# Optimization experiments

Measured on AMD Instinct MI355X. Metric: run time of the kernel, lower is better.

## Reference

```python
import jax, jax.numpy as jnp
from jax import lax
import numpy as np

B, H, W_, C, F = 4, 32, 32, 16, 16
KH, KW = 3, 3
L = 1.0


def setup_inputs() -> dict:
    key = jax.random.key(0)
    k1, k2, k3, k4 = jax.random.split(key, 4)
    inputs = jax.random.normal(k1, (B, H, W_, C), dtype=jnp.float32)
    # lecun_normal-style scales (stddev = 1/sqrt(fan_in))
    m_scale = 1.0 / np.sqrt(H * W_ * 1)
    g_scale = 1.0 / np.sqrt(KH * KW * C)
    M = jax.random.normal(k2, (H, W_, 1, H, W_, 1), dtype=jnp.float32) * m_scale
    Wp = jax.random.normal(k3, (H, W_, 1, H, W_, 1), dtype=jnp.float32) * m_scale
    G = jax.random.normal(k4, (H, W_, KH, KW, C, F), dtype=jnp.float32) * g_scale
    return {"inputs": inputs, "M": M, "Wp": Wp, "G": G}


def reference(inputs, M, Wp, G):
    b, h, w, c = inputs.shape
    kh, kw, f = G.shape[2], G.shape[3], G.shape[5]
    M2 = M[:, :, 0, :, :, 0]   # (i,j,p,q)
    W2 = Wp[:, :, 0, :, :, 0]  # (i,j,p,q)
    # first_term[b,i,j,c] = sum_pq M[i,j,p,q] * inputs[b,p,q,c]
    first = jnp.einsum('ijpq,bpqc->bijc', M2, inputs)
    # One big conv: kernel (kh,kw,c, h*w*f) gives shifted for every output pixel (i,j)
    K = jnp.transpose(G, (2, 3, 4, 0, 1, 5)).reshape(kh, kw, c, h * w * f)
    shifted = lax.conv_general_dilated(
        inputs, K, window_strides=(1, 1), padding='SAME',
        dimension_numbers=('NHWC', 'HWIO', 'NHWC'))
    shifted = shifted.reshape(b, h, w, h, w, f)  # (b,p,q,i,j,f)
    diff = jax.nn.relu(inputs[:, :, :, None, None, :] - shifted)  # (b,p,q,i,j,c)
    # second_term[b,i,j,c] = sum_pq W[i,j,p,q] * relu(inputs - shifted)[b,p,q,i,j,c]
    second = jnp.einsum('ijpq,bpqijc->bijc', W2, diff)
    return first - L * second
```

## Files before the change

### kernel.cpp

```cpp
#include <hip/hip_runtime.h>


typedef __attribute__((ext_vector_type(8))) short bf16x8;
typedef __attribute__((ext_vector_type(4))) float f32x4;

__device__ inline unsigned short f2bf(float x) {
    unsigned u = __float_as_uint(x);
    u += 0x7FFFu + ((u >> 16) & 1u);
    return (unsigned short)(u >> 16);
}
__device__ inline unsigned pack2(float a, float b) {
    return (unsigned)f2bf(a) | ((unsigned)f2bf(b) << 16);
}

template<bool XF>
__global__ __launch_bounds__(256) void build_A(const float* __restrict__ inp,
                                               uint4* __restrict__ A,
                                               float4* __restrict__ Xf) {
    const int tid = blockIdx.x * 256 + threadIdx.x;
    const int u = tid >> 12;
    if (XF && u >= 20) {
        const int idx = tid - 81920;
        const int tile = idx >> 6;
        const int ll = idx & 63;
        const int rowb = tile * 16 + (ll >> 4) * 4;
        const int col = ll & 15;
        float4 v;
        v.x = inp[(rowb + 0) * 16 + col];
        v.y = inp[(rowb + 1) * 16 + col];
        v.z = inp[(rowb + 2) * 16 + col];
        v.w = inp[(rowb + 3) * 16 + col];
        Xf[idx] = v;
        return;
    }
    const int row = tid & 4095;
    const int tile = row >> 4, m = row & 15;
    if (u >= 18) {
        const uint4 z = {0, 0, 0, 0};
        A[(tile * 5 + 4) * 64 + (u - 16) * 16 + m] = z;
        return;
    }
    const int tap = u >> 1, h = u & 1;
    const int dh = tap / 3, dw = tap - dh * 3;
    const int b = row >> 10, pq = row & 1023;
    const int p = pq >> 5, q = pq & 31;
    const int pp = p + dh - 1, qq = q + dw - 1;
    const int kk = tap >> 1, quad = (tap & 1) * 2 + h;
    uint4 o = {0, 0, 0, 0};
    if (((unsigned)pp < 32u) && ((unsigned)qq < 32u)) {
        const float4* s = (const float4*)(inp + b * 16384 + (pp * 32 + qq) * 16 + 8 * h);
        const float4 f0 = s[0], f1 = s[1];
        o.x = pack2(f0.x, f0.y); o.y = pack2(f0.z, f0.w);
        o.z = pack2(f1.x, f1.y); o.w = pack2(f1.z, f1.w);
    }
    A[(tile * 5 + kk) * 64 + quad * 16 + m] = o;
}

template<bool XF>
__global__ __launch_bounds__(512, 2) void inrf_main(
    const float* __restrict__ inp,
    const float* __restrict__ M,
    const float* __restrict__ Wp,
    const float* __restrict__ G,
    const uint4* __restrict__ Aw,
    const float4* __restrict__ Xf,
    float* __restrict__ out)
{
    const int bid = blockIdx.x;
    const int t = threadIdx.x;

    __shared__ __align__(16) float W2l[4096];
    __shared__ __align__(16) float M2l[4096];
    __shared__ float red[8][64];

    {
        const float* Wg = Wp + bid * 4096;
        const float* Mg = M  + bid * 4096;
#pragma unroll
        for (int i = 0; i < 8; ++i) {
            W2l[t + i * 512] = Wg[t + i * 512];
            M2l[t + i * 512] = Mg[t + i * 512];
        }
    }

    const int l = t & 63, w = t >> 6;
    const int quad = l >> 4, col = l & 15;
    const int b = w >> 1;

    const float* Gg = G + bid * 9216;
    bf16x8 Bf[4][5];
#pragma unroll
    for (int ij = 0; ij < 4; ++ij) {
#pragma unroll
        for (int kk = 0; kk < 5; ++kk) {
            bf16x8 f;
#pragma unroll
            for (int j = 0; j < 8; ++j) {
                const int k = kk * 32 + quad * 8 + j;
                const float v = (k < 144) ? Gg[ij * 2304 + k * 16 + col] : 0.f;
                f[j] = (short)f2bf(v);
            }
            Bf[ij][kk] = f;
        }
    }

    __syncthreads();

    const int tile0 = b * 64 + (w & 1) * 32;
    const float* inb = inp + b * 16384;
    (void)inb;

    float accv[4] = {0.f, 0.f, 0.f, 0.f};

    uint4 A0[5], A1[5];
    float4 v0, v1;

    auto prefetch = [&](uint4 (&Ar)[5], float4& vr, int tn) {
#pragma unroll
        for (int kk = 0; kk < 5; ++kk) Ar[kk] = Aw[(tn * 5 + kk) * 64 + l];
        if (XF) {
            vr = Xf[tn * 64 + l];
        } else {
            const int pqb = (tn & 63) * 16 + quad * 4;
            vr.x = inb[(pqb + 0) * 16 + col];
            vr.y = inb[(pqb + 1) * 16 + col];
            vr.z = inb[(pqb + 2) * 16 + col];
            vr.w = inb[(pqb + 3) * 16 + col];
        }
    };

    auto compute = [&](const uint4 (&Ar)[5], const float4& vr, int tg) {
        f32x4 C[4];
#pragma unroll
        for (int ij = 0; ij < 4; ++ij) C[ij] = (f32x4){0.f, 0.f, 0.f, 0.f};
#pragma unroll
        for (int kk = 0; kk < 5; ++kk) {
            const bf16x8 a = __builtin_bit_cast(bf16x8, Ar[kk]);
#pragma unroll
            for (int ij = 0; ij < 4; ++ij)
                C[ij] = __builtin_amdgcn_mfma_f32_16x16x32_bf16(a, Bf[ij][kk], C[ij], 0, 0, 0);
        }
        const int pqb = (tg & 63) * 16 + quad * 4;
#pragma unroll
        for (int ij = 0; ij < 4; ++ij) {
            const float4 w2 = *(const float4*)&W2l[ij * 1024 + pqb];
            const float4 m2 = *(const float4*)&M2l[ij * 1024 + pqb];
            accv[ij] += m2.x * vr.x - w2.x * fmaxf(vr.x - C[ij][0], 0.f);
            accv[ij] += m2.y * vr.y - w2.y * fmaxf(vr.y - C[ij][1], 0.f);
            accv[ij] += m2.z * vr.z - w2.z * fmaxf(vr.z - C[ij][2], 0.f);
            accv[ij] += m2.w * vr.w - w2.w * fmaxf(vr.w - C[ij][3], 0.f);
        }
    };

    prefetch(A0, v0, tile0);
#pragma unroll 1
    for (int i = 0; i < 32; i += 2) {
        prefetch(A1, v1, tile0 + i + 1);
        compute(A0, v0, tile0 + i);
        if (i + 2 < 32) prefetch(A0, v0, tile0 + i + 2);
        compute(A1, v1, tile0 + i + 1);
    }

#pragma unroll
    for (int ij = 0; ij < 4; ++ij) {
        float v = accv[ij];
        v += __shfl_xor(v, 16);
        v += __shfl_xor(v, 32);
        if (l < 16) red[w][ij * 16 + l] = v;
    }
    __syncthreads();

    if (t < 256) {
        const int ob = t >> 6, oij = (t >> 4) & 3, oc = t & 15;
        const float r0 = red[ob * 2][oij * 16 + oc] + red[ob * 2 + 1][oij * 16 + oc];
        out[ob * 16384 + (bid * 4 + oij) * 16 + oc] = r0;
    }
}

extern "C" void kernel_launch(void* const* d_in, const int* in_sizes, int n_in,
                              void* d_out, int out_size, void* d_ws, size_t ws_size,
                              hipStream_t stream) {
    const float* inp = (const float*)d_in[0];
    const float* M   = (const float*)d_in[1];
    const float* Wp  = (const float*)d_in[2];
    const float* G   = (const float*)d_in[3];
    float* out = (float*)d_out;

    uint4*  A  = (uint4*)d_ws;
    float4* Xf = (float4*)((char*)d_ws + 81920 * sizeof(uint4));
    const size_t need = 81920 * sizeof(uint4) + 16384 * sizeof(float4);

    if (ws_size >= need) {
        build_A<true><<<dim3(384), dim3(256), 0, stream>>>(inp, A, Xf);
        inrf_main<true><<<dim3(256), dim3(512), 0, stream>>>(inp, M, Wp, G, A, Xf, out);
    } else {
        build_A<false><<<dim3(320), dim3(256), 0, stream>>>(inp, A, nullptr);
        inrf_main<false><<<dim3(256), dim3(512), 0, stream>>>(inp, M, Wp, G, A, nullptr, out);
    }
}
```

Baseline: 98.31 us.

## Repartition work: blocks own ij-slices and tile groups, stage A via LDS, atomic reduce

Each block now handles 64 output pixels (8 per wave) across a group of 16 pq-tiles, rather than 4 pixels across all tiles. Shared A tiles and input values are double-buffered in LDS with global_load_lds, so all 8 waves reuse them instead of each loading from global. M and Wp are read straight from global rather than staged in LDS. Partial sums go to out with atomicAdd, so build_A now zeroes the output first. The workspace-size fallback path is dropped. The atomics and the doubled B-fragment register footprint may reduce occupancy or add contention.

```diff
diff --git a/kernel.cpp b/kernel.cpp
--- a/kernel.cpp
+++ b/kernel.cpp
@@ -13,13 +13,22 @@
     return (unsigned)f2bf(a) | ((unsigned)f2bf(b) << 16);
 }
 
-template<bool XF>
+__device__ inline void gld_lds16(const void* g, void* l) {
+    __builtin_amdgcn_global_load_lds((const __attribute__((address_space(1))) void*)g,
+                                     (__attribute__((address_space(3))) void*)l, 16, 0, 0);
+}
+
 __global__ __launch_bounds__(256) void build_A(const float* __restrict__ inp,
                                                uint4* __restrict__ A,
-                                               float4* __restrict__ Xf) {
+                                               float4* __restrict__ Xf,
+                                               float4* __restrict__ outz) {
     const int tid = blockIdx.x * 256 + threadIdx.x;
     const int u = tid >> 12;
-    if (XF && u >= 20) {
+    if (u >= 24) {
+        outz[tid - 98304] = (float4){0.f, 0.f, 0.f, 0.f};
+        return;
+    }
+    if (u >= 20) {
         const int idx = tid - 81920;
         const int tile = idx >> 6;
         const int ll = idx & 63;
@@ -56,9 +65,7 @@
     A[(tile * 5 + kk) * 64 + quad * 16 + m] = o;
 }
 
-template<bool XF>
 __global__ __launch_bounds__(512, 2) void inrf_main(
-    const float* __restrict__ inp,
     const float* __restrict__ M,
     const float* __restrict__ Wp,
     const float* __restrict__ G,
@@ -67,113 +74,106 @@
     float* __restrict__ out)
 {
     const int bid = blockIdx.x;
-    const int t = threadIdx.x;
+    const int ijblk = bid & 15;
+    const int tgrp  = bid >> 4;
+    const int tile0 = tgrp * 16;
+    const int bb    = tile0 >> 6;
 
-    __shared__ __align__(16) float W2l[4096];
-    __shared__ __align__(16) float M2l[4096];
-    __shared__ float red[8][64];
+    const int t = threadIdx.x, l = t & 63, w = t >> 6;
+    const int quad = l >> 4, col = l & 15;
 
-    {
-        const float* Wg = Wp + bid * 4096;
-        const float* Mg = M  + bid * 4096;
+    __shared__ __align__(16) uint4  Ab[2][4][5][64];
+    __shared__ __align__(16) float4 Xb[2][4][64];
+
+    auto stage = [&](int buf, int ct0) {
 #pragma unroll
-        for (int i = 0; i < 8; ++i) {
-            W2l[t + i * 512] = Wg[t + i * 512];
-            M2l[t + i * 512] = Mg[t + i * 512];
+        for (int r = 0; r < 3; ++r) {
+            const int s = w * 3 + r;
+            if (s < 20) {
+                const int ct = s / 5, kk = s - ct * 5;
+                gld_lds16(&Aw[((ct0 + ct) * 5 + kk) * 64 + l], &Ab[buf][ct][kk][0]);
+            } else {
+                const int ct = s - 20;
+                gld_lds16(&Xf[(ct0 + ct) * 64 + l], &Xb[buf][ct][0]);
+            }
         }
-    }
+    };
 
-    const int l = t & 63, w = t >> 6;
-    const int quad = l >> 4, col = l & 15;
-    const int b = w >> 1;
+    stage(0, tile0);
 
-    const float* Gg = G + bid * 9216;
-    bf16x8 Bf[4][5];
+    const int ij0 = ijblk * 64 + w * 8;
+    bf16x8 Bf[8][5];
 #pragma unroll
-    for (int ij = 0; ij < 4; ++ij) {
+    for (int ij = 0; ij < 8; ++ij) {
+        const float* Gg = G + (ij0 + ij) * 2304;
 #pragma unroll
         for (int kk = 0; kk < 5; ++kk) {
             bf16x8 f;
 #pragma unroll
             for (int j = 0; j < 8; ++j) {
                 const int k = kk * 32 + quad * 8 + j;
-                const float v = (k < 144) ? Gg[ij * 2304 + k * 16 + col] : 0.f;
+                const float v = (k < 144) ? Gg[k * 16 + col] : 0.f;
                 f[j] = (short)f2bf(v);
             }
             Bf[ij][kk] = f;
         }
     }
 
+    float accv[8] = {0.f, 0.f, 0.f, 0.f, 0.f, 0.f, 0.f, 0.f};
+
+    asm volatile("s_waitcnt vmcnt(0)" ::: "memory");
     __syncthreads();
 
-    const int tile0 = b * 64 + (w & 1) * 32;
-    const float* inb = inp + b * 16384;
-    (void)inb;
-
-    float accv[4] = {0.f, 0.f, 0.f, 0.f};
-
-    uint4 A0[5], A1[5];
-    float4 v0, v1;
-
-    auto prefetch = [&](uint4 (&Ar)[5], float4& vr, int tn) {
+    int buf = 0;
+#pragma unroll 1
+    for (int ph = 0; ph < 4; ++ph) {
+        if (ph < 3) stage(buf ^ 1, tile0 + (ph + 1) * 4);
 #pragma unroll
-        for (int kk = 0; kk < 5; ++kk) Ar[kk] = Aw[(tn * 5 + kk) * 64 + l];
-        if (XF) {
-            vr = Xf[tn * 64 + l];
-        } else {
-            const int pqb = (tn & 63) * 16 + quad * 4;
-            vr.x = inb[(pqb + 0) * 16 + col];
-            vr.y = inb[(pqb + 1) * 16 + col];
-            vr.z = inb[(pqb + 2) * 16 + col];
-            vr.w = inb[(pqb + 3) * 16 + col];
+        for (int ct = 0; ct < 4; ++ct) {
+            const int tg = tile0 + ph * 4 + ct;
+            uint4 Af[5];
+#pragma unroll
+            for (int kk = 0; kk < 5; ++kk) Af[kk] = Ab[buf][ct][kk][l];
+            const float4 vr = Xb[buf][ct][l];
+            const int pqb = (tg & 63) * 16 + quad * 4;
+#pragma unroll
+            for (int h = 0; h < 2; ++h) {
+                f32x4 C[4];
+#pragma unroll
+                for (int jj = 0; jj < 4; ++jj) C[jj] = (f32x4){0.f, 0.f, 0.f, 0.f};
+#pragma unroll
+                for (int kk = 0; kk < 5; ++kk) {
+                    const bf16x8 a = __builtin_bit_cast(bf16x8, Af[kk]);
+#pragma unroll
+                    for (int jj = 0; jj < 4; ++jj)
+                        C[jj] = __builtin_amdgcn_mfma_f32_16x16x32_bf16(
+                                    a, Bf[h * 4 + jj][kk], C[jj], 0, 0, 0);
+                }
+#pragma unroll
+                for (int jj = 0; jj < 4; ++jj) {
+                    const int ijg = ij0 + h * 4 + jj;
+                    const float4 w2 = *(const float4*)&Wp[ijg * 1024 + pqb];
+                    const float4 m2 = *(const float4*)&M [ijg * 1024 + pqb];
+                    float a0 = accv[h * 4 + jj];
+                    a0 += m2.x * vr.x - w2.x * fmaxf(vr.x - C[jj][0], 0.f);
+                    a0 += m2.y * vr.y - w2.y * fmaxf(vr.y - C[jj][1], 0.f);
+                    a0 += m2.z * vr.z - w2.z * fmaxf(vr.z - C[jj][2], 0.f);
+                    a0 += m2.w * vr.w - w2.w * fmaxf(vr.w - C[jj][3], 0.f);
+                    accv[h * 4 + jj] = a0;
+                }
+            }
         }
-    };
-
-    auto compute = [&](const uint4 (&Ar)[5], const float4& vr, int tg) {
-        f32x4 C[4];
-#pragma unroll
-        for (int ij = 0; ij < 4; ++ij) C[ij] = (f32x4){0.f, 0.f, 0.f, 0.f};
-#pragma unroll
-        for (int kk = 0; kk < 5; ++kk) {
-            const bf16x8 a = __builtin_bit_cast(bf16x8, Ar[kk]);
-#pragma unroll
-            for (int ij = 0; ij < 4; ++ij)
-                C[ij] = __builtin_amdgcn_mfma_f32_16x16x32_bf16(a, Bf[ij][kk], C[ij], 0, 0, 0);
-        }
-        const int pqb = (tg & 63) * 16 + quad * 4;
-#pragma unroll
-        for (int ij = 0; ij < 4; ++ij) {
-            const float4 w2 = *(const float4*)&W2l[ij * 1024 + pqb];
-            const float4 m2 = *(const float4*)&M2l[ij * 1024 + pqb];
-            accv[ij] += m2.x * vr.x - w2.x * fmaxf(vr.x - C[ij][0], 0.f);
-            accv[ij] += m2.y * vr.y - w2.y * fmaxf(vr.y - C[ij][1], 0.f);
-            accv[ij] += m2.z * vr.z - w2.z * fmaxf(vr.z - C[ij][2], 0.f);
-            accv[ij] += m2.w * vr.w - w2.w * fmaxf(vr.w - C[ij][3], 0.f);
-        }
-    };
-
-    prefetch(A0, v0, tile0);
-#pragma unroll 1
-    for (int i = 0; i < 32; i += 2) {
-        prefetch(A1, v1, tile0 + i + 1);
-        compute(A0, v0, tile0 + i);
-        if (i + 2 < 32) prefetch(A0, v0, tile0 + i + 2);
-        compute(A1, v1, tile0 + i + 1);
+        asm volatile("s_waitcnt vmcnt(0)" ::: "memory");
+        __syncthreads();
+        buf ^= 1;
     }
 
 #pragma unroll
-    for (int ij = 0; ij < 4; ++ij) {
+    for (int ij = 0; ij < 8; ++ij) {
         float v = accv[ij];
         v += __shfl_xor(v, 16);
         v += __shfl_xor(v, 32);
-        if (l < 16) red[w][ij * 16 + l] = v;
-    }
-    __syncthreads();
-
-    if (t < 256) {
-        const int ob = t >> 6, oij = (t >> 4) & 3, oc = t & 15;
-        const float r0 = red[ob * 2][oij * 16 + oc] + red[ob * 2 + 1][oij * 16 + oc];
-        out[ob * 16384 + (bid * 4 + oij) * 16 + oc] = r0;
+        if (l < 16) atomicAdd(&out[bb * 16384 + (ij0 + ij) * 16 + l], v);
     }
 }
 
@@ -188,13 +188,7 @@
 
     uint4*  A  = (uint4*)d_ws;
     float4* Xf = (float4*)((char*)d_ws + 81920 * sizeof(uint4));
-    const size_t need = 81920 * sizeof(uint4) + 16384 * sizeof(float4);
 
-    if (ws_size >= need) {
-        build_A<true><<<dim3(384), dim3(256), 0, stream>>>(inp, A, Xf);
-        inrf_main<true><<<dim3(256), dim3(512), 0, stream>>>(inp, M, Wp, G, A, Xf, out);
-    } else {
-        build_A<false><<<dim3(320), dim3(256), 0, stream>>>(inp, A, nullptr);
-        inrf_main<false><<<dim3(256), dim3(512), 0, stream>>>(inp, M, Wp, G, A, nullptr, out);
-    }
+    build_A<<<dim3(448), dim3(256), 0, stream>>>(inp, A, Xf, (float4*)out);
+    inrf_main<<<dim3(256), dim3(512), 0, stream>>>(M, Wp, G, A, Xf, out);
 }
```

Measured after the change: 328.3 us. 234% more time.
